# Performance work log

Measured on AMD Instinct MI355X. Metric: run time of the kernel, lower is better.

## Reference

```python
import jax, jax.numpy as jnp
import numpy as np

B, T, C = 4, 2048, 2048
H, D = 16, 128  # n_heads, head_dim


def _rope_freqs(seq_len, head_dim, base=10000.0):
    half = head_dim // 2
    inv = 1.0 / (base ** (np.arange(half, dtype=np.float32) / half))
    t = np.arange(seq_len, dtype=np.float32)
    ang = np.outer(t, inv)  # (T, D/2)
    return jnp.asarray(np.stack([np.cos(ang), np.sin(ang)], axis=-1))  # (T, D/2, 2)


def setup_inputs() -> dict:
    key = jax.random.key(0)
    k1, k2, k3 = jax.random.split(key, 3)
    x = jax.random.normal(k1, (B, T, C), dtype=jnp.float32)
    freqs = _rope_freqs(T, D)
    # additive causal mask
    mask = jnp.where(jnp.tril(jnp.ones((T, T), dtype=bool)), 0.0, -1e9).astype(jnp.float32)
    w_qkv = jax.random.normal(k2, (3 * C, C), dtype=jnp.float32) * (1.0 / np.sqrt(C))
    w_out = jax.random.normal(k3, (C, C), dtype=jnp.float32) * (1.0 / np.sqrt(C))
    return {"x": x, "freqs": freqs, "mask": mask, "w_qkv": w_qkv, "w_out": w_out}


def apply_rope(x, freqs):
    # x: (B,H,T,D), freqs: (T,D/2,2)
    xr = x.reshape(*x.shape[:-1], -1, 2)
    cos, sin = freqs[..., 0], freqs[..., 1]
    x0, x1 = xr[..., 0], xr[..., 1]
    rot = jnp.stack([x0 * cos - x1 * sin, x0 * sin + x1 * cos], axis=-1)
    return rot.reshape(x.shape)


def reference(x, freqs, mask, w_qkv, w_out):
    b, t, c = x.shape
    qkv = jnp.einsum('btc,fc->btf', x, w_qkv).reshape(b, t, 3, H, D)
    q, k, v = jnp.moveaxis(qkv, 2, 0)          # each (b,t,H,D)
    q = jnp.transpose(q, (0, 2, 1, 3))          # (b,H,t,D)
    k = jnp.transpose(k, (0, 2, 1, 3))
    v = jnp.transpose(v, (0, 2, 1, 3))
    q = apply_rope(q, freqs[:t])
    k = apply_rope(k, freqs[:t])
    scale = 1.0 / np.sqrt(D).astype(np.float32)
    attn = jnp.einsum('bhqd,bhkd->bhqk', q, k) * scale + mask[:t, :t]
    attn = jax.nn.softmax(attn, axis=-1)
    out = jnp.einsum('bhqk,bhkd->bhqd', attn, v)
    out = jnp.transpose(out, (0, 2, 1, 3)).reshape(b, t, c)
    return jnp.einsum('btc,fc->btf', out, w_out)
```

## Files before the change

kernel.cpp:

```cpp
#include <hip/hip_runtime.h>

typedef unsigned short u16;
typedef unsigned int   u32;

using sx8   = __attribute__((ext_vector_type(8))) short;
using f32x4 = __attribute__((ext_vector_type(4))) float;
using u16x8 = __attribute__((ext_vector_type(8))) unsigned short;

#define BB 4
#define TT 2048
#define CC 2048
#define HH 16
#define DD 128
#define FF 6144
#define MM 8192

static __device__ __forceinline__ u16 f2bf(float f) {
    u32 u = __builtin_bit_cast(u32, f);
    u32 lsb = (u >> 16) & 1u;
    u += 0x7fffu + lsb;
    return (u16)(u >> 16);
}
static __device__ __forceinline__ float bf2f(u16 b) {
    return __builtin_bit_cast(float, (u32)b << 16);
}
static __device__ __forceinline__ f32x4 mfma16(sx8 a, sx8 b, f32x4 c) {
    return __builtin_amdgcn_mfma_f32_16x16x32_bf16(a, b, c, 0, 0, 0);
}
static __device__ __forceinline__ u32 pkbf(float a, float b) {
    return (u32)f2bf(a) | ((u32)f2bf(b) << 16);
}

__global__ __launch_bounds__(256) void k_cvt(const float* __restrict__ src,
                                             u16* __restrict__ dst, int n8) {
    int i = blockIdx.x * 256 + threadIdx.x;
    if (i >= n8) return;
    const float4* s = (const float4*)src;
    float4 a = s[2 * (size_t)i], b = s[2 * (size_t)i + 1];
    u16x8 r;
    r[0] = f2bf(a.x); r[1] = f2bf(a.y); r[2] = f2bf(a.z); r[3] = f2bf(a.w);
    r[4] = f2bf(b.x); r[5] = f2bf(b.y); r[6] = f2bf(b.z); r[7] = f2bf(b.w);
    *(u16x8*)(dst + 8 * (size_t)i) = r;
}

template <int OUTF32>
__global__ __launch_bounds__(256, 2) void k_gemm(const u16* __restrict__ A,
                                                 const u16* __restrict__ Bt,
                                                 float* __restrict__ Cf,
                                                 u16* __restrict__ Cb,
                                                 int M, int N, int K) {
    __shared__ __align__(16) u16 sA[128 * 32];
    __shared__ __align__(16) u16 sB[128 * 32];
    const int n0 = blockIdx.x * 128, m0 = blockIdx.y * 128;
    const int tid = threadIdx.x, w = tid >> 6, l = tid & 63;
    const int wm = w >> 1, wn = w & 1;
    const int lr = l & 15, lg = l >> 4;
    f32x4 acc[4][4] = {};

    const int idx0 = w * 128 + l;
    const int idx1 = idx0 + 64;
    const int ra0 = idx0 >> 2, ca0 = (idx0 & 3) * 8;
    const int ra1 = idx1 >> 2, ca1 = (idx1 & 3) * 8;
    const u16* Ar0 = A + (size_t)(m0 + ra0) * K + ca0;
    const u16* Ar1 = A + (size_t)(m0 + ra1) * K + ca1;
    const u16* Br0 = Bt + (size_t)(n0 + ra0) * K + ca0;
    const u16* Br1 = Bt + (size_t)(n0 + ra1) * K + ca1;
    u16* sAd0 = sA + (w * 2 + 0) * 512;
    u16* sAd1 = sA + (w * 2 + 1) * 512;
    u16* sBd0 = sB + (w * 2 + 0) * 512;
    u16* sBd1 = sB + (w * 2 + 1) * 512;

    for (int k0 = 0; k0 < K; k0 += 32) {
        __builtin_amdgcn_global_load_lds(
            (const __attribute__((address_space(1))) void*)(Ar0 + k0),
            (__attribute__((address_space(3))) void*)sAd0, 16, 0, 0);
        __builtin_amdgcn_global_load_lds(
            (const __attribute__((address_space(1))) void*)(Ar1 + k0),
            (__attribute__((address_space(3))) void*)sAd1, 16, 0, 0);
        __builtin_amdgcn_global_load_lds(
            (const __attribute__((address_space(1))) void*)(Br0 + k0),
            (__attribute__((address_space(3))) void*)sBd0, 16, 0, 0);
        __builtin_amdgcn_global_load_lds(
            (const __attribute__((address_space(1))) void*)(Br1 + k0),
            (__attribute__((address_space(3))) void*)sBd1, 16, 0, 0);
        __syncthreads();
        sx8 af[4], bfr[4];
#pragma unroll
        for (int i = 0; i < 4; i++)
            af[i] = *(const sx8*)(sA + (wm * 64 + i * 16 + lr) * 32 + lg * 8);
#pragma unroll
        for (int j = 0; j < 4; j++)
            bfr[j] = *(const sx8*)(sB + (wn * 64 + j * 16 + lr) * 32 + lg * 8);
#pragma unroll
        for (int i = 0; i < 4; i++)
#pragma unroll
            for (int j = 0; j < 4; j++)
                acc[i][j] = mfma16(af[i], bfr[j], acc[i][j]);
        __syncthreads();
    }
#pragma unroll
    for (int i = 0; i < 4; i++) {
        const int mr = m0 + wm * 64 + i * 16 + lg * 4;
#pragma unroll
        for (int j = 0; j < 4; j++) {
            const int nc = n0 + wn * 64 + j * 16 + lr;
#pragma unroll
            for (int rg = 0; rg < 4; rg++) {
                float v = acc[i][j][rg];
                size_t off = (size_t)(mr + rg) * N + nc;
                if (OUTF32) Cf[off] = v;
                else        Cb[off] = f2bf(v);
            }
        }
    }
}

__global__ __launch_bounds__(256) void k_rope(const u16* __restrict__ qkv,
                                              const float* __restrict__ freqs,
                                              u16* __restrict__ Qo,
                                              u16* __restrict__ Ko,
                                              u16* __restrict__ Vt) {
    const int t0 = blockIdx.x * 64, h = blockIdx.y, b = blockIdx.z;
    const int tid = threadIdx.x;
    const float scale = 0.08838834764831845f;
    __shared__ u16 vt[64][129];
#pragma unroll
    for (int it = 0; it < 16; ++it) {
        int idx = tid + it * 256;
        int trow = idx >> 6, pr = idx & 63;
        int t = t0 + trow;
        size_t ib = (size_t)(b * TT + t) * FF + h * DD + 2 * pr;
        float2 cs = *(const float2*)(freqs + (size_t)t * DD + 2 * pr);
        size_t ob = ((size_t)(b * HH + h) * TT + t) * DD + 2 * pr;
        {
            u32 qp = *(const u32*)(qkv + ib);
            float x0 = bf2f((u16)(qp & 0xffff)), x1 = bf2f((u16)(qp >> 16));
            u32 r = (u32)f2bf((x0 * cs.x - x1 * cs.y) * scale) |
                    ((u32)f2bf((x0 * cs.y + x1 * cs.x) * scale) << 16);
            *(u32*)(Qo + ob) = r;
        }
        {
            u32 kp = *(const u32*)(qkv + ib + CC);
            float x0 = bf2f((u16)(kp & 0xffff)), x1 = bf2f((u16)(kp >> 16));
            u32 r = (u32)f2bf(x0 * cs.x - x1 * cs.y) |
                    ((u32)f2bf(x0 * cs.y + x1 * cs.x) << 16);
            *(u32*)(Ko + ob) = r;
        }
        {
            u32 vp = *(const u32*)(qkv + ib + 2 * CC);
            vt[trow][2 * pr]     = (u16)(vp & 0xffff);
            vt[trow][2 * pr + 1] = (u16)(vp >> 16);
        }
    }
    __syncthreads();
    const size_t vb = (size_t)(b * HH + h) * DD * TT + t0;
#pragma unroll
    for (int it = 0; it < 32; ++it) {
        int idx = tid + it * 256;
        int d = idx >> 6, tr = idx & 63;
        Vt[vb + (size_t)d * TT + tr] = vt[tr][d];
    }
}

#define KV 64
#define PST 68

__global__ __launch_bounds__(256, 2) void k_attn(const u16* __restrict__ Q,
                                                 const u16* __restrict__ K,
                                                 const u16* __restrict__ Vt,
                                                 u16* __restrict__ AO) {
    const int fid = blockIdx.x + 8 * blockIdx.y + 128 * blockIdx.z;
    const int xg = fid >> 6;
    const int hb = fid & 63;
    const int h = hb & 15, b = hb >> 4;

    const int tid = threadIdx.x, w = tid >> 6, l = tid & 63;
    const int lr = l & 15, lg = l >> 4;
    const size_t bh = (size_t)(b * HH + h);
    const u16* Qh = Q + bh * TT * DD;
    const u16* Kh = K + bh * TT * DD;
    const u16* Vh = Vt + bh * DD * TT;

    __shared__ __align__(16) u16 sK[2][KV * DD];
    __shared__ __align__(16) u16 sP[4][32 * PST];
    u16* myP = sP[w];

    const int strow = tid >> 4;
    const int sc16  = tid & 15;

    for (int rep = 0; rep < 2; ++rep) {
        const int g = rep ? (15 - xg) : xg;
        const int q0w = g * 128 + w * 32;
        const int nt = 2 * g + 2;

        sx8 qf[2][4];
#pragma unroll
        for (int i = 0; i < 2; i++)
#pragma unroll
            for (int kk = 0; kk < 4; kk++)
                qf[i][kk] = *(const sx8*)(Qh + (size_t)(q0w + i * 16 + lr) * DD + kk * 32 + lg * 8);

        f32x4 o[2][8] = {};
        float mrow[2] = {-1e30f, -1e30f};
        float lrow[2] = {0.0f, 0.0f};

#pragma unroll
        for (int i = 0; i < 4; ++i) {
            const int row = i * 16 + strow;
            const int scol = (sc16 ^ (row & 7)) * 8;
            __builtin_amdgcn_global_load_lds(
                (const __attribute__((address_space(1))) void*)(Kh + (size_t)row * DD + scol),
                (__attribute__((address_space(3))) void*)(&sK[0][i * 2048 + w * 512]),
                16, 0, 0);
        }
        __syncthreads();

        int cur = 0;
        for (int t = 0; t < nt; ++t) {
            const int k0 = t * KV;
            if (t + 1 < nt) {
                const int kn = k0 + KV;
#pragma unroll
                for (int i = 0; i < 4; ++i) {
                    const int row = i * 16 + strow;
                    const int scol = (sc16 ^ (row & 7)) * 8;
                    __builtin_amdgcn_global_load_lds(
                        (const __attribute__((address_space(1))) void*)(Kh + (size_t)(kn + row) * DD + scol),
                        (__attribute__((address_space(3))) void*)(&sK[cur ^ 1][i * 2048 + w * 512]),
                        16, 0, 0);
                }
            }
            if (k0 <= q0w) {
                f32x4 st[2][4] = {};
#pragma unroll
                for (int j = 0; j < 4; ++j) {
                    const int row = j * 16 + lr;
                    const int rx = row & 7;
                    sx8 kf[4];
#pragma unroll
                    for (int kk = 0; kk < 4; ++kk) {
                        const int c16 = (kk * 4 + lg) ^ rx;
                        kf[kk] = *(const sx8*)(&sK[cur][row * DD + c16 * 8]);
                    }
#pragma unroll
                    for (int kk = 0; kk < 4; ++kk) {
                        st[0][j] = mfma16(kf[kk], qf[0][kk], st[0][j]);
                        st[1][j] = mfma16(kf[kk], qf[1][kk], st[1][j]);
                    }
                }
                sx8 vf0[8];
#pragma unroll
                for (int n = 0; n < 8; ++n)
                    vf0[n] = *(const sx8*)(Vh + (size_t)(n * 16 + lr) * TT + k0 + lg * 8);

                const bool need_mask = (k0 + 63 > q0w);
                const int klocal = lg * 4;
#pragma unroll
                for (int i = 0; i < 2; ++i) {
                    if (need_mask) {
                        const int cl = q0w + i * 16 + lr - k0;
#pragma unroll
                        for (int j = 0; j < 4; ++j)
#pragma unroll
                            for (int rg = 0; rg < 4; ++rg)
                                if (j * 16 + klocal + rg > cl) st[i][j][rg] = -1e30f;
                    }
                    f32x4 m4;
#pragma unroll
                    for (int rg = 0; rg < 4; ++rg)
                        m4[rg] = fmaxf(fmaxf(st[i][0][rg], st[i][1][rg]),
                                       fmaxf(st[i][2][rg], st[i][3][rg]));
                    float pm = fmaxf(fmaxf(m4[0], m4[1]), fmaxf(m4[2], m4[3]));
                    pm = fmaxf(pm, __shfl_xor(pm, 16));
                    pm = fmaxf(pm, __shfl_xor(pm, 32));
                    const float mold = mrow[i];
                    const bool resc = pm > mold + 8.0f;
                    const float mnew = resc ? pm : mold;
                    mrow[i] = mnew;
                    float rs = 0.0f;
#pragma unroll
                    for (int j = 0; j < 4; ++j) {
                        float p0 = __expf(st[i][j][0] - mnew);
                        float p1 = __expf(st[i][j][1] - mnew);
                        float p2 = __expf(st[i][j][2] - mnew);
                        float p3 = __expf(st[i][j][3] - mnew);
                        rs += (p0 + p1) + (p2 + p3);
                        *(uint2*)(myP + (i * 16 + lr) * PST + j * 16 + klocal) =
                            make_uint2(pkbf(p0, p1), pkbf(p2, p3));
                    }
                    rs += __shfl_xor(rs, 16);
                    rs += __shfl_xor(rs, 32);
                    const float sf = resc ? __expf(mold - mnew) : 1.0f;
                    lrow[i] = lrow[i] * sf + rs;
                    if (__any(resc)) {
                        f32x4 sfo;
#pragma unroll
                        for (int rg = 0; rg < 4; ++rg)
                            sfo[rg] = __shfl(sf, 4 * lg + rg);
#pragma unroll
                        for (int n = 0; n < 8; ++n) o[i][n] *= sfo;
                    }
                }
                asm volatile("s_waitcnt lgkmcnt(0)" ::: "memory");
                __builtin_amdgcn_sched_barrier(0);

                sx8 pa0[2], pa1[2];
                pa0[0] = *(const sx8*)(myP + (size_t)lr * PST + lg * 8);
                pa0[1] = *(const sx8*)(myP + (size_t)(16 + lr) * PST + lg * 8);
                pa1[0] = *(const sx8*)(myP + (size_t)lr * PST + 32 + lg * 8);
                pa1[1] = *(const sx8*)(myP + (size_t)(16 + lr) * PST + 32 + lg * 8);
#pragma unroll
                for (int n = 0; n < 8; ++n) {
                    o[0][n] = mfma16(pa0[0], vf0[n], o[0][n]);
                    o[1][n] = mfma16(pa0[1], vf0[n], o[1][n]);
                }
#pragma unroll
                for (int n = 0; n < 8; ++n) {
                    sx8 vf1 = *(const sx8*)(Vh + (size_t)(n * 16 + lr) * TT + k0 + 32 + lg * 8);
                    o[0][n] = mfma16(pa1[0], vf1, o[0][n]);
                    o[1][n] = mfma16(pa1[1], vf1, o[1][n]);
                }
            }
            __syncthreads();
            cur ^= 1;
        }

#pragma unroll
        for (int i = 0; i < 2; ++i) {
            f32x4 linv;
#pragma unroll
            for (int rg = 0; rg < 4; ++rg)
                linv[rg] = __shfl(lrow[i], 4 * lg + rg);
#pragma unroll
            for (int rg = 0; rg < 4; ++rg) {
                const float inv = 1.0f / linv[rg];
                const int tq = q0w + i * 16 + lg * 4 + rg;
                u16* orow = AO + ((size_t)(b * TT) + tq) * CC + h * DD + lr;
#pragma unroll
                for (int n = 0; n < 8; ++n)
                    orow[n * 16] = f2bf(o[i][n][rg] * inv);
            }
        }
    }
}

extern "C" void kernel_launch(void* const* d_in, const int* in_sizes, int n_in,
                              void* d_out, int out_size, void* d_ws, size_t ws_size,
                              hipStream_t stream) {
    const float* x     = (const float*)d_in[0];
    const float* freqs = (const float*)d_in[1];
    const float* w_qkv = (const float*)d_in[3];
    const float* w_out = (const float*)d_in[4];
    float* out = (float*)d_out;

    u16* ws   = (u16*)d_ws;
    u16* xb   = ws;
    u16* wqb  = xb   + (size_t)MM * CC;
    u16* wob  = wqb  + (size_t)FF * CC;
    u16* qkvb = wob  + (size_t)CC * CC;
    u16* Qr   = qkvb + (size_t)MM * FF;
    u16* Kr   = Qr   + (size_t)MM * CC;
    u16* Vt   = Kr   + (size_t)MM * CC;
    u16* AO   = qkvb;

    k_cvt<<<MM * CC / 2048, 256, 0, stream>>>(x, xb, MM * CC / 8);
    k_cvt<<<FF * CC / 2048, 256, 0, stream>>>(w_qkv, wqb, FF * CC / 8);
    k_cvt<<<CC * CC / 2048, 256, 0, stream>>>(w_out, wob, CC * CC / 8);

    k_gemm<0><<<dim3(FF / 128, MM / 128), 256, 0, stream>>>(xb, wqb, nullptr, qkvb, MM, FF, CC);
    k_rope<<<dim3(TT / 64, HH, BB), 256, 0, stream>>>(qkvb, freqs, Qr, Kr, Vt);
    k_attn<<<dim3(8, HH, BB), 256, 0, stream>>>(Qr, Kr, Vt, AO);
    k_gemm<1><<<dim3(CC / 128, MM / 128), 256, 0, stream>>>(AO, wob, out, nullptr, MM, CC, CC);
}
```

Baseline: 544.3 us.

## Rewrite GEMM with 256x256 tiles, 4-stage LDS pipeline, swizzle and XCD remap

The GEMM kernel now uses 512-thread blocks computing 256x256 output tiles. It stages K-slices through a four-buffer LDS ring using async global-to-LDS loads, with explicit waitcnt and barriers so loads run ahead of the MFMAs. It also XOR-swizzles the LDS layout to reduce bank conflicts and remaps block IDs across the 8 XCDs for L2 locality. The aim is to hide memory latency and raise MFMA utilisation in both projections, at the cost of 128 KB of LDS per block, higher register pressure and hand-tuned synchronisation that could be fragile.

```diff
diff --git a/kernel.cpp b/kernel.cpp
--- a/kernel.cpp
+++ b/kernel.cpp
@@ -44,69 +44,109 @@
 }
 
 template <int OUTF32>
-__global__ __launch_bounds__(256, 2) void k_gemm(const u16* __restrict__ A,
+__global__ __launch_bounds__(512, 2) void k_gemm(const u16* __restrict__ A,
                                                  const u16* __restrict__ Bt,
                                                  float* __restrict__ Cf,
                                                  u16* __restrict__ Cb,
                                                  int M, int N, int K) {
-    __shared__ __align__(16) u16 sA[128 * 32];
-    __shared__ __align__(16) u16 sB[128 * 32];
-    const int n0 = blockIdx.x * 128, m0 = blockIdx.y * 128;
+    __shared__ __align__(16) u16 sA[4][256 * 32];
+    __shared__ __align__(16) u16 sB[4][256 * 32];
+    const int nbn = N >> 8;
+    const int nwg = (M >> 8) * nbn;
+    const int cpx = nwg >> 3;
+    const int fid = blockIdx.x;
+    const int sid = (fid & 7) * cpx + (fid >> 3);
+    const int m0 = (sid / nbn) << 8, n0 = (sid % nbn) << 8;
+
     const int tid = threadIdx.x, w = tid >> 6, l = tid & 63;
-    const int wm = w >> 1, wn = w & 1;
+    const int wm = w >> 2, wn = w & 3;
     const int lr = l & 15, lg = l >> 4;
-    f32x4 acc[4][4] = {};
-
-    const int idx0 = w * 128 + l;
-    const int idx1 = idx0 + 64;
-    const int ra0 = idx0 >> 2, ca0 = (idx0 & 3) * 8;
-    const int ra1 = idx1 >> 2, ca1 = (idx1 & 3) * 8;
-    const u16* Ar0 = A + (size_t)(m0 + ra0) * K + ca0;
-    const u16* Ar1 = A + (size_t)(m0 + ra1) * K + ca1;
-    const u16* Br0 = Bt + (size_t)(n0 + ra0) * K + ca0;
-    const u16* Br1 = Bt + (size_t)(n0 + ra1) * K + ca1;
-    u16* sAd0 = sA + (w * 2 + 0) * 512;
-    u16* sAd1 = sA + (w * 2 + 1) * 512;
-    u16* sBd0 = sB + (w * 2 + 0) * 512;
-    u16* sBd1 = sB + (w * 2 + 1) * 512;
-
-    for (int k0 = 0; k0 < K; k0 += 32) {
-        __builtin_amdgcn_global_load_lds(
-            (const __attribute__((address_space(1))) void*)(Ar0 + k0),
-            (__attribute__((address_space(3))) void*)sAd0, 16, 0, 0);
-        __builtin_amdgcn_global_load_lds(
-            (const __attribute__((address_space(1))) void*)(Ar1 + k0),
-            (__attribute__((address_space(3))) void*)sAd1, 16, 0, 0);
-        __builtin_amdgcn_global_load_lds(
-            (const __attribute__((address_space(1))) void*)(Br0 + k0),
-            (__attribute__((address_space(3))) void*)sBd0, 16, 0, 0);
-        __builtin_amdgcn_global_load_lds(
-            (const __attribute__((address_space(1))) void*)(Br1 + k0),
-            (__attribute__((address_space(3))) void*)sBd1, 16, 0, 0);
-        __syncthreads();
-        sx8 af[4], bfr[4];
-#pragma unroll
-        for (int i = 0; i < 4; i++)
-            af[i] = *(const sx8*)(sA + (wm * 64 + i * 16 + lr) * 32 + lg * 8);
-#pragma unroll
-        for (int j = 0; j < 4; j++)
-            bfr[j] = *(const sx8*)(sB + (wn * 64 + j * 16 + lr) * 32 + lg * 8);
-#pragma unroll
-        for (int i = 0; i < 4; i++)
-#pragma unroll
-            for (int j = 0; j < 4; j++)
-                acc[i][j] = mfma16(af[i], bfr[j], acc[i][j]);
-        __syncthreads();
-    }
-#pragma unroll
-    for (int i = 0; i < 4; i++) {
-        const int mr = m0 + wm * 64 + i * 16 + lg * 4;
-#pragma unroll
-        for (int j = 0; j < 4; j++) {
-            const int nc = n0 + wn * 64 + j * 16 + lr;
-#pragma unroll
-            for (int rg = 0; rg < 4; rg++) {
-                float v = acc[i][j][rg];
+    const int nk = K >> 5;
+
+    const int srow = tid >> 2;
+    const int sg   = tid & 3;
+    const int ssg  = sg ^ ((srow >> 1) & 3);
+    const u16* pA0 = A  + (size_t)(m0 + srow)       * K + ssg * 8;
+    const u16* pA1 = A  + (size_t)(m0 + srow + 128) * K + ssg * 8;
+    const u16* pB0 = Bt + (size_t)(n0 + srow)       * K + ssg * 8;
+    const u16* pB1 = Bt + (size_t)(n0 + srow + 128) * K + ssg * 8;
+    const int dst0 = w * 512;
+
+    const int gA = lg ^ ((lr >> 1) & 3);
+    const int raOff = (wm * 128 + lr) * 32 + gA * 8;
+    const int rbOff = (wn * 64 + lr) * 32 + gA * 8;
+
+    f32x4 acc[8][4] = {};
+
+#define GLL(SRC, DST) __builtin_amdgcn_global_load_lds( \
+        (const __attribute__((address_space(1))) void*)(SRC), \
+        (__attribute__((address_space(3))) void*)(DST), 16, 0, 0)
+
+#pragma unroll
+    for (int kt = 0; kt < 3; ++kt) {
+        GLL(pA0 + kt * 32, &sA[kt][dst0]);
+        GLL(pA1 + kt * 32, &sA[kt][4096 + dst0]);
+        GLL(pB0 + kt * 32, &sB[kt][dst0]);
+        GLL(pB1 + kt * 32, &sB[kt][4096 + dst0]);
+    }
+
+#pragma unroll 1
+    for (int kt = 0; kt < nk; ++kt) {
+        asm volatile("s_waitcnt lgkmcnt(0)" ::: "memory");
+        if (kt + 2 < nk)      asm volatile("s_waitcnt vmcnt(8)" ::: "memory");
+        else if (kt + 1 < nk) asm volatile("s_waitcnt vmcnt(4)" ::: "memory");
+        else                  asm volatile("s_waitcnt vmcnt(0)" ::: "memory");
+        __builtin_amdgcn_sched_barrier(0);
+        __builtin_amdgcn_s_barrier();
+        __builtin_amdgcn_sched_barrier(0);
+        const u16* bufA = sA[kt & 3];
+        const u16* bufB = sB[kt & 3];
+        const bool stg = (kt + 3) < nk;
+        const int bw = (kt + 3) & 3;
+        if (stg) {
+            GLL(pA0 + (kt + 3) * 32, &sA[bw][dst0]);
+            GLL(pA1 + (kt + 3) * 32, &sA[bw][4096 + dst0]);
+        }
+        sx8 af[4], bf[4];
+#pragma unroll
+        for (int mi = 0; mi < 4; ++mi) af[mi] = *(const sx8*)(bufA + raOff + mi * 512);
+#pragma unroll
+        for (int ni = 0; ni < 4; ++ni) bf[ni] = *(const sx8*)(bufB + rbOff + ni * 512);
+        __builtin_amdgcn_s_setprio(1);
+#pragma unroll
+        for (int mi = 0; mi < 4; ++mi)
+#pragma unroll
+            for (int ni = 0; ni < 4; ++ni)
+                acc[mi][ni] = mfma16(af[mi], bf[ni], acc[mi][ni]);
+        __builtin_amdgcn_s_setprio(0);
+        __builtin_amdgcn_s_barrier();
+        __builtin_amdgcn_sched_barrier(0);
+        if (stg) {
+            GLL(pB0 + (kt + 3) * 32, &sB[bw][dst0]);
+            GLL(pB1 + (kt + 3) * 32, &sB[bw][4096 + dst0]);
+        }
+        sx8 ag[4];
+#pragma unroll
+        for (int mi = 0; mi < 4; ++mi) ag[mi] = *(const sx8*)(bufA + raOff + (mi + 4) * 512);
+        __builtin_amdgcn_s_setprio(1);
+#pragma unroll
+        for (int mi = 0; mi < 4; ++mi)
+#pragma unroll
+            for (int ni = 0; ni < 4; ++ni)
+                acc[mi + 4][ni] = mfma16(ag[mi], bf[ni], acc[mi + 4][ni]);
+        __builtin_amdgcn_s_setprio(0);
+    }
+#undef GLL
+
+#pragma unroll
+    for (int mi = 0; mi < 8; ++mi) {
+        const int mr = m0 + wm * 128 + mi * 16 + lg * 4;
+#pragma unroll
+        for (int ni = 0; ni < 4; ++ni) {
+            const int nc = n0 + wn * 64 + ni * 16 + lr;
+#pragma unroll
+            for (int rg = 0; rg < 4; ++rg) {
+                float v = acc[mi][ni][rg];
                 size_t off = (size_t)(mr + rg) * N + nc;
                 if (OUTF32) Cf[off] = v;
                 else        Cb[off] = f2bf(v);
@@ -367,8 +407,8 @@
     k_cvt<<<FF * CC / 2048, 256, 0, stream>>>(w_qkv, wqb, FF * CC / 8);
     k_cvt<<<CC * CC / 2048, 256, 0, stream>>>(w_out, wob, CC * CC / 8);
 
-    k_gemm<0><<<dim3(FF / 128, MM / 128), 256, 0, stream>>>(xb, wqb, nullptr, qkvb, MM, FF, CC);
+    k_gemm<0><<<(MM / 256) * (FF / 256), 512, 0, stream>>>(xb, wqb, nullptr, qkvb, MM, FF, CC);
     k_rope<<<dim3(TT / 64, HH, BB), 256, 0, stream>>>(qkvb, freqs, Qr, Kr, Vt);
     k_attn<<<dim3(8, HH, BB), 256, 0, stream>>>(Qr, Kr, Vt, AO);
-    k_gemm<1><<<dim3(CC / 128, MM / 128), 256, 0, stream>>>(AO, wob, out, nullptr, MM, CC, CC);
-}
+    k_gemm<1><<<(MM / 256) * (CC / 256), 512, 0, stream>>>(AO, wob, out, nullptr, MM, CC, CC);
+}
```

Measured after the change: 532.0 us. 1.02x faster.

## Fuse RoPE, Q scaling and V transpose into QKV GEMM epilogue

Applied to the files above, without the earlier changes.

Removes the separate RoPE kernel and the intermediate bf16 QKV buffer. The QKV GEMM epilogue now applies the rotary embedding through a lane shuffle to get the paired element, scales Q, and writes Q/K in head-major layout. V is transposed through a small per-warp LDS tile into the Vt layout. This saves a full write and read of the QKV tensor and one launch, at the cost of scattered 2-byte stores and extra LDS in the GEMM, which may hurt occupancy.

```diff
diff --git a/kernel.cpp b/kernel.cpp
--- a/kernel.cpp
+++ b/kernel.cpp
@@ -43,14 +43,18 @@
     *(u16x8*)(dst + 8 * (size_t)i) = r;
 }
 
-template <int OUTF32>
+template <int MODE>
 __global__ __launch_bounds__(256, 2) void k_gemm(const u16* __restrict__ A,
                                                  const u16* __restrict__ Bt,
                                                  float* __restrict__ Cf,
-                                                 u16* __restrict__ Cb,
+                                                 const float* __restrict__ freqs,
+                                                 u16* __restrict__ Qo,
+                                                 u16* __restrict__ Ko,
+                                                 u16* __restrict__ Vt,
                                                  int M, int N, int K) {
     __shared__ __align__(16) u16 sA[128 * 32];
     __shared__ __align__(16) u16 sB[128 * 32];
+    __shared__ __align__(16) u16 vT[4][64][17];
     const int n0 = blockIdx.x * 128, m0 = blockIdx.y * 128;
     const int tid = threadIdx.x, w = tid >> 6, l = tid & 63;
     const int wm = w >> 1, wn = w & 1;
@@ -98,67 +102,71 @@
                 acc[i][j] = mfma16(af[i], bfr[j], acc[i][j]);
         __syncthreads();
     }
-#pragma unroll
-    for (int i = 0; i < 4; i++) {
-        const int mr = m0 + wm * 64 + i * 16 + lg * 4;
-#pragma unroll
-        for (int j = 0; j < 4; j++) {
-            const int nc = n0 + wn * 64 + j * 16 + lr;
-#pragma unroll
-            for (int rg = 0; rg < 4; rg++) {
-                float v = acc[i][j][rg];
-                size_t off = (size_t)(mr + rg) * N + nc;
-                if (OUTF32) Cf[off] = v;
-                else        Cb[off] = f2bf(v);
-            }
-        }
-    }
-}
-
-__global__ __launch_bounds__(256) void k_rope(const u16* __restrict__ qkv,
-                                              const float* __restrict__ freqs,
-                                              u16* __restrict__ Qo,
-                                              u16* __restrict__ Ko,
-                                              u16* __restrict__ Vt) {
-    const int t0 = blockIdx.x * 64, h = blockIdx.y, b = blockIdx.z;
-    const int tid = threadIdx.x;
-    const float scale = 0.08838834764831845f;
-    __shared__ u16 vt[64][129];
-#pragma unroll
-    for (int it = 0; it < 16; ++it) {
-        int idx = tid + it * 256;
-        int trow = idx >> 6, pr = idx & 63;
-        int t = t0 + trow;
-        size_t ib = (size_t)(b * TT + t) * FF + h * DD + 2 * pr;
-        float2 cs = *(const float2*)(freqs + (size_t)t * DD + 2 * pr);
-        size_t ob = ((size_t)(b * HH + h) * TT + t) * DD + 2 * pr;
-        {
-            u32 qp = *(const u32*)(qkv + ib);
-            float x0 = bf2f((u16)(qp & 0xffff)), x1 = bf2f((u16)(qp >> 16));
-            u32 r = (u32)f2bf((x0 * cs.x - x1 * cs.y) * scale) |
-                    ((u32)f2bf((x0 * cs.y + x1 * cs.x) * scale) << 16);
-            *(u32*)(Qo + ob) = r;
-        }
-        {
-            u32 kp = *(const u32*)(qkv + ib + CC);
-            float x0 = bf2f((u16)(kp & 0xffff)), x1 = bf2f((u16)(kp >> 16));
-            u32 r = (u32)f2bf(x0 * cs.x - x1 * cs.y) |
-                    ((u32)f2bf(x0 * cs.y + x1 * cs.x) << 16);
-            *(u32*)(Ko + ob) = r;
-        }
-        {
-            u32 vp = *(const u32*)(qkv + ib + 2 * CC);
-            vt[trow][2 * pr]     = (u16)(vp & 0xffff);
-            vt[trow][2 * pr + 1] = (u16)(vp >> 16);
-        }
-    }
-    __syncthreads();
-    const size_t vb = (size_t)(b * HH + h) * DD * TT + t0;
-#pragma unroll
-    for (int it = 0; it < 32; ++it) {
-        int idx = tid + it * 256;
-        int d = idx >> 6, tr = idx & 63;
-        Vt[vb + (size_t)d * TT + tr] = vt[tr][d];
+
+    if (MODE == 1) {
+#pragma unroll
+        for (int i = 0; i < 4; i++) {
+            const int mr = m0 + wm * 64 + i * 16 + lg * 4;
+#pragma unroll
+            for (int j = 0; j < 4; j++) {
+                const int nc = n0 + wn * 64 + j * 16 + lr;
+#pragma unroll
+                for (int rg = 0; rg < 4; rg++)
+                    Cf[(size_t)(mr + rg) * N + nc] = acc[i][j][rg];
+            }
+        }
+    } else {
+        const int b = m0 >> 11;
+        const int t0blk = m0 & 2047;
+        const int kind = n0 >> 11;
+        const int h = (n0 & 2047) >> 7;
+        const size_t bh = (size_t)(b * HH + h);
+        if (kind < 2) {
+            u16* dst = (kind == 0 ? Qo : Ko) + bh * (size_t)(TT * DD);
+            const float qs = (kind == 0) ? 0.08838834764831845f : 1.0f;
+#pragma unroll
+            for (int i = 0; i < 4; i++) {
+#pragma unroll
+                for (int j = 0; j < 4; j++) {
+                    const int d = wn * 64 + j * 16 + lr;
+                    const int dp2 = (d >> 1) * 2;
+#pragma unroll
+                    for (int rg = 0; rg < 4; rg++) {
+                        const int t = t0blk + wm * 64 + i * 16 + lg * 4 + rg;
+                        float v = acc[i][j][rg];
+                        float p = __shfl_xor(v, 1);
+                        float2 cs = *(const float2*)(freqs + (size_t)t * DD + dp2);
+                        float r = (lr & 1) ? (p * cs.y + v * cs.x)
+                                           : (v * cs.x - p * cs.y);
+                        dst[(size_t)t * DD + d] = f2bf(r * qs);
+                    }
+                }
+            }
+        } else {
+            u16* dstV = Vt + bh * (size_t)(DD * TT);
+            const int t0w = t0blk + wm * 64;
+            const int dl = l >> 2, seg = l & 3;
+#pragma unroll
+            for (int j = 0; j < 4; ++j) {
+#pragma unroll
+                for (int i = 0; i < 4; ++i)
+#pragma unroll
+                    for (int rg = 0; rg < 4; ++rg)
+                        vT[w][i * 16 + lg * 4 + rg][lr] = f2bf(acc[i][j][rg]);
+                asm volatile("s_waitcnt lgkmcnt(0)" ::: "memory");
+                __builtin_amdgcn_sched_barrier(0);
+                u16x8 t2[2];
+#pragma unroll
+                for (int jj = 0; jj < 16; ++jj)
+                    t2[jj >> 3][jj & 7] = vT[w][seg * 16 + jj][dl];
+                const int dg = wn * 64 + j * 16 + dl;
+                u16* orow = dstV + (size_t)dg * TT + t0w + seg * 16;
+                *(u16x8*)orow = t2[0];
+                *((u16x8*)orow + 1) = t2[1];
+                asm volatile("s_waitcnt lgkmcnt(0)" ::: "memory");
+                __builtin_amdgcn_sched_barrier(0);
+            }
+        }
     }
 }
 
@@ -357,18 +365,18 @@
     u16* xb   = ws;
     u16* wqb  = xb   + (size_t)MM * CC;
     u16* wob  = wqb  + (size_t)FF * CC;
-    u16* qkvb = wob  + (size_t)CC * CC;
-    u16* Qr   = qkvb + (size_t)MM * FF;
+    u16* AO   = wob  + (size_t)CC * CC;
+    u16* Qr   = AO   + (size_t)MM * CC;
     u16* Kr   = Qr   + (size_t)MM * CC;
     u16* Vt   = Kr   + (size_t)MM * CC;
-    u16* AO   = qkvb;
 
     k_cvt<<<MM * CC / 2048, 256, 0, stream>>>(x, xb, MM * CC / 8);
     k_cvt<<<FF * CC / 2048, 256, 0, stream>>>(w_qkv, wqb, FF * CC / 8);
     k_cvt<<<CC * CC / 2048, 256, 0, stream>>>(w_out, wob, CC * CC / 8);
 
-    k_gemm<0><<<dim3(FF / 128, MM / 128), 256, 0, stream>>>(xb, wqb, nullptr, qkvb, MM, FF, CC);
-    k_rope<<<dim3(TT / 64, HH, BB), 256, 0, stream>>>(qkvb, freqs, Qr, Kr, Vt);
+    k_gemm<2><<<dim3(FF / 128, MM / 128), 256, 0, stream>>>(
+        xb, wqb, nullptr, freqs, Qr, Kr, Vt, MM, FF, CC);
     k_attn<<<dim3(8, HH, BB), 256, 0, stream>>>(Qr, Kr, Vt, AO);
-    k_gemm<1><<<dim3(CC / 128, MM / 128), 256, 0, stream>>>(AO, wob, out, nullptr, MM, CC, CC);
-}
+    k_gemm<1><<<dim3(CC / 128, MM / 128), 256, 0, stream>>>(
+        AO, wob, out, nullptr, nullptr, nullptr, nullptr, MM, CC, CC);
+}
```

After: 520.4 us. 4.4% less time.
